# Kernel tuning notes

Measured on AMD Instinct MI355X. Metric: run time of the kernel, lower is better.

Reference implementation:

```python
import jax, jax.numpy as jnp
import numpy as np

N = 50000   # nodes
E = 1600000 # edges
D = 128     # feature dim (in = hidden = 128)


def setup_inputs() -> dict:
    key = jax.random.key(0)
    k1, k2, k3, k4 = jax.random.split(key, 4)
    scale = 1.0 / np.sqrt(D)
    return {
        "x": jax.random.normal(k1, (N, D), jnp.float32),
        "edge_index": jax.random.randint(k2, (2, E), 0, N, dtype=jnp.int32),
        "W0": jax.random.normal(k3, (D, D), jnp.float32) * scale,
        "b0": jnp.zeros((D,), jnp.float32),
        "W1": jax.random.normal(k4, (D, D), jnp.float32) * scale,
        "b1": jnp.zeros((D,), jnp.float32),
    }


def _gcn_norm(edge_index, num_nodes):
    # Add self-loops, compute symmetric normalization D^-1/2 A_hat D^-1/2.
    loop = jnp.arange(num_nodes, dtype=edge_index.dtype)
    src = jnp.concatenate([edge_index[0], loop])
    dst = jnp.concatenate([edge_index[1], loop])
    deg = jax.ops.segment_sum(jnp.ones_like(dst, jnp.float32), dst,
                              num_segments=num_nodes)
    dinv = jnp.where(deg > 0, jax.lax.rsqrt(deg), 0.0)
    norm = dinv[dst] * dinv[src]  # [E+N]
    return src, dst, norm


def _gcn_layer(x, src, dst, norm, W, b, num_nodes):
    h = x @ W                                  # [N, D]
    msg = h[src] * norm[:, None]               # gather + scale  [E+N, D]
    out = jax.ops.segment_sum(msg, dst, num_segments=num_nodes)  # scatter-add
    return out + b


def reference(x, edge_index, W0, b0, W1, b1):
    num_nodes = x.shape[0]
    src, dst, norm = _gcn_norm(edge_index, num_nodes)
    # forward loops over the first k=2 convs, ReLU after each (as in source)
    x = jax.nn.relu(_gcn_layer(x, src, dst, norm, W0, b0, num_nodes))
    x = jax.nn.relu(_gcn_layer(x, src, dst, norm, W1, b1, num_nodes))
    return x
```

## Files before the change

kernel.cpp:

```cpp
#include <hip/hip_runtime.h>
#include <hip/hip_bf16.h>

#define D 128
#define CHUNK 8192
#define SPAN_CAP 768


typedef __attribute__((ext_vector_type(8))) short short8;
typedef __attribute__((ext_vector_type(4))) float floatx4;

static __device__ inline unsigned int f2bf(float f) {
    unsigned int u = __float_as_uint(f);
    return (u + 0x7FFFu + ((u >> 16) & 1u)) >> 16;
}
static __device__ inline float bflo(unsigned int u) { return __uint_as_float(u << 16); }
static __device__ inline float bfhi(unsigned int u) { return __uint_as_float(u & 0xFFFF0000u); }

__global__ __launch_bounds__(256) void k01_swz_hist(const float* __restrict__ W0,
                                                    const float* __restrict__ W1,
                                                    short8* __restrict__ whi0, short8* __restrict__ wlo0,
                                                    short8* __restrict__ whi1, short8* __restrict__ wlo1,
                                                    const int* __restrict__ dst,
                                                    int* __restrict__ blockhist, int E_) {
    __shared__ int h[256];
    const int tid = threadIdx.x;
    if (blockIdx.x < 16) {
        int gid = blockIdx.x * 256 + tid;
        const float* W = (gid < 2048) ? W0 : W1;
        short8* whi = (gid < 2048) ? whi0 : whi1;
        short8* wlo = (gid < 2048) ? wlo0 : wlo1;
        int t2 = gid & 2047;
        int t = t2 >> 8, q = (t2 >> 6) & 3, lane = t2 & 63;
        short8 hi, lo;
        #pragma unroll
        for (int j = 0; j < 8; ++j) {
            int k = q * 32 + (lane >> 4) * 8 + j;
            int n = t * 16 + (lane & 15);
            float w = W[k * D + n];
            unsigned int hh = f2bf(w);
            hi[j] = (short)hh;
            lo[j] = (short)f2bf(w - __uint_as_float(hh << 16));
        }
        whi[t2] = hi;
        wlo[t2] = lo;
    } else {
        const int b = blockIdx.x - 16;
        h[tid] = 0;
        __syncthreads();
        const int e0 = b * CHUNK;
        const int e1 = min(E_, e0 + CHUNK);
        for (int e = e0 + tid; e < e1; e += 256)
            atomicAdd(&h[dst[e] >> 8], 1);
        __syncthreads();
        blockhist[b * 256 + tid] = h[tid];
    }
}

__global__ __launch_bounds__(256) void k23_scan_scatter(const int* __restrict__ blockhist,
                                                        const int* __restrict__ dst,
                                                        const int* __restrict__ src,
                                                        int* __restrict__ bucket_offs,
                                                        unsigned int* __restrict__ buf,
                                                        int NB, int NBUK, int E_) {
    __shared__ int s[256];
    __shared__ int c[256];
    const int myb = blockIdx.x, tid = threadIdx.x;
    int total = 0, prefix = 0;
    #pragma unroll 4
    for (int b2 = 0; b2 < NB; ++b2) {
        int t = blockhist[b2 * 256 + tid];
        total += t;
        prefix += (b2 < myb) ? t : 0;
    }
    s[tid] = total;
    __syncthreads();
    #pragma unroll
    for (int off = 1; off < 256; off <<= 1) {
        int x = (tid >= off) ? s[tid - off] : 0;
        __syncthreads();
        s[tid] += x;
        __syncthreads();
    }
    int bstart = s[tid] - total;
    if (myb == 0) {
        if (tid < NBUK) bucket_offs[tid] = bstart;
        if (tid == 0) bucket_offs[NBUK] = E_;
    }
    c[tid] = bstart + prefix;
    __syncthreads();

    const int e0 = myb * CHUNK;
    const int e1 = min(E_, e0 + CHUNK);
    for (int e = e0 + tid; e < e1; e += 256) {
        int v = dst[e];
        int sdx = src[e];
        int pos = atomicAdd(&c[v >> 8], 1);
        buf[pos] = (unsigned int)sdx | ((unsigned int)(v & 255) << 16);
    }
}

__global__ __launch_bounds__(256) void k4_bucket(const unsigned int* __restrict__ buf,
                                                 const int* __restrict__ bucket_offs,
                                                 int* __restrict__ offs,
                                                 float* __restrict__ dinv,
                                                 int* __restrict__ col, int N_, int E_) {
    __shared__ int h[256];
    __shared__ int s[256];
    __shared__ int c[256];
    const int beta = blockIdx.x, tid = threadIdx.x;
    const int start = bucket_offs[beta];
    const int end   = bucket_offs[beta + 1];

    h[tid] = 0;
    __syncthreads();
    for (int e = start + tid; e < end; e += 256)
        atomicAdd(&h[(buf[e] >> 16) & 255], 1);
    __syncthreads();

    int deg = h[tid];
    s[tid] = deg;
    __syncthreads();
    #pragma unroll
    for (int off = 1; off < 256; off <<= 1) {
        int x = (tid >= off) ? s[tid - off] : 0;
        __syncthreads();
        s[tid] += x;
        __syncthreads();
    }
    int excl = s[tid] - deg;

    int v0 = beta * 256 + tid;
    if (v0 < N_) {
        offs[v0] = start + excl;
        dinv[v0] = rsqrtf((float)(deg + 1));
    }
    if (beta == 0 && tid == 0) offs[N_] = E_;
    c[tid] = start + excl;
    __syncthreads();

    for (int e = start + tid; e < end; e += 256) {
        unsigned int p = buf[e];
        int pos = atomicAdd(&c[(p >> 16) & 255], 1);
        col[pos] = (int)(p & 0xFFFFu);
    }
}

__global__ __launch_bounds__(256) void gemm_mfma(const float* __restrict__ A,
                                                 const short8* __restrict__ whi,
                                                 const short8* __restrict__ wlo,
                                                 const float* __restrict__ dinv,
                                                 unsigned int* __restrict__ Gu, int nrows) {
    __shared__ float tileT[128][65];

    const int tid  = threadIdx.x;
    const int wave = tid >> 6, lane = tid & 63;
    const int m = lane & 15, quad = lane >> 4;
    const int rowInBlk = wave * 16;
    const int arow = min(blockIdx.x * 64 + rowInBlk + m, nrows - 1);
    const float* Ap = A + (size_t)arow * D + quad * 8;

    floatx4 acc[8];
    #pragma unroll
    for (int t = 0; t < 8; ++t) acc[t] = (floatx4){0.f, 0.f, 0.f, 0.f};

    #pragma unroll
    for (int q = 0; q < 4; ++q) {
        float4 a0 = *(const float4*)(Ap + q * 32);
        float4 a1 = *(const float4*)(Ap + q * 32 + 4);
        float av[8] = {a0.x, a0.y, a0.z, a0.w, a1.x, a1.y, a1.z, a1.w};
        short8 ahi, alo;
        #pragma unroll
        for (int j = 0; j < 8; ++j) {
            unsigned int h = f2bf(av[j]);
            ahi[j] = (short)h;
            alo[j] = (short)f2bf(av[j] - __uint_as_float(h << 16));
        }
        #pragma unroll
        for (int t = 0; t < 8; ++t) {
            short8 bh = whi[(t * 4 + q) * 64 + lane];
            short8 bl = wlo[(t * 4 + q) * 64 + lane];
            acc[t] = __builtin_amdgcn_mfma_f32_16x16x32_bf16(ahi, bh, acc[t], 0, 0, 0);
            acc[t] = __builtin_amdgcn_mfma_f32_16x16x32_bf16(alo, bh, acc[t], 0, 0, 0);
            acc[t] = __builtin_amdgcn_mfma_f32_16x16x32_bf16(ahi, bl, acc[t], 0, 0, 0);
        }
    }

    #pragma unroll
    for (int t = 0; t < 8; ++t)
        #pragma unroll
        for (int r = 0; r < 4; ++r)
            tileT[t * 16 + m][rowInBlk + quad * 4 + r] = acc[t][r];
    __syncthreads();

    const int orow = tid >> 2, seg = tid & 3;
    const int grow = blockIdx.x * 64 + orow;
    if (grow < nrows) {
        float s = dinv[grow];
        const int p = seg >> 1;
        unsigned int* Gp = Gu + ((size_t)(p * nrows + grow)) * 32 + (seg & 1) * 16;
        #pragma unroll
        for (int i = 0; i < 4; ++i) {
            int c0 = seg * 32 + i * 8;
            uint4 o4;
            o4.x = f2bf(tileT[c0 + 0][orow] * s) | (f2bf(tileT[c0 + 1][orow] * s) << 16);
            o4.y = f2bf(tileT[c0 + 2][orow] * s) | (f2bf(tileT[c0 + 3][orow] * s) << 16);
            o4.z = f2bf(tileT[c0 + 4][orow] * s) | (f2bf(tileT[c0 + 5][orow] * s) << 16);
            o4.w = f2bf(tileT[c0 + 6][orow] * s) | (f2bf(tileT[c0 + 7][orow] * s) << 16);
            ((uint4*)Gp)[i] = o4;
        }
    }
}

__global__ __launch_bounds__(256) void aggregate_kernel(const unsigned int* __restrict__ Gu,
                                                        const int* __restrict__ offs,
                                                        const int* __restrict__ col,
                                                        const float* __restrict__ dinv,
                                                        const float* __restrict__ bias,
                                                        float* __restrict__ out, int nnodes,
                                                        int ngroups) {
    __shared__ int scol[SPAN_CAP];
    __shared__ int soffs[9];
    const int bid   = blockIdx.x;
    const int xcd   = bid & 7;
    const int plane = xcd >> 2;
    const int i     = (bid >> 3) * 4 + (xcd & 3);
    if (i >= ngroups) return;
    const int tid   = threadIdx.x;
    const int node0 = i * 8;

    if (tid < 9) soffs[tid] = offs[min(node0 + tid, nnodes)];
    __syncthreads();
    const int s0   = soffs[0];
    const int span = soffs[8] - s0;
    const bool lds_ok = (span <= SPAN_CAP);
    if (lds_ok) {
        for (int k = tid; k < span; k += 256) scol[k] = col[s0 + k];
    }
    __syncthreads();

    const int lane = tid & 31;
    const int node = node0 + (tid >> 5);
    if (node >= nnodes) return;
    const unsigned int* P = Gu + (size_t)plane * nnodes * 32;

    unsigned int su = P[(size_t)node * 32 + lane];
    float ax = bflo(su), ay = bfhi(su);

    const int s = soffs[tid >> 5];
    const int e = soffs[(tid >> 5) + 1];
    int idx = s;

    if (lds_ok) {
        const int b0 = s - s0;
        int k = 0;
        const int deg = e - s;
        for (; k + 8 <= deg; k += 8) {
            int j0 = scol[b0 + k + 0], j1 = scol[b0 + k + 1], j2 = scol[b0 + k + 2], j3 = scol[b0 + k + 3];
            int j4 = scol[b0 + k + 4], j5 = scol[b0 + k + 5], j6 = scol[b0 + k + 6], j7 = scol[b0 + k + 7];
            unsigned int u0 = P[(size_t)j0 * 32 + lane];
            unsigned int u1 = P[(size_t)j1 * 32 + lane];
            unsigned int u2 = P[(size_t)j2 * 32 + lane];
            unsigned int u3 = P[(size_t)j3 * 32 + lane];
            unsigned int u4 = P[(size_t)j4 * 32 + lane];
            unsigned int u5 = P[(size_t)j5 * 32 + lane];
            unsigned int u6 = P[(size_t)j6 * 32 + lane];
            unsigned int u7 = P[(size_t)j7 * 32 + lane];
            ax += ((bflo(u0) + bflo(u1)) + (bflo(u2) + bflo(u3))) +
                  ((bflo(u4) + bflo(u5)) + (bflo(u6) + bflo(u7)));
            ay += ((bfhi(u0) + bfhi(u1)) + (bfhi(u2) + bfhi(u3))) +
                  ((bfhi(u4) + bfhi(u5)) + (bfhi(u6) + bfhi(u7)));
        }
        for (; k + 4 <= deg; k += 4) {
            int j0 = scol[b0 + k + 0], j1 = scol[b0 + k + 1], j2 = scol[b0 + k + 2], j3 = scol[b0 + k + 3];
            unsigned int u0 = P[(size_t)j0 * 32 + lane];
            unsigned int u1 = P[(size_t)j1 * 32 + lane];
            unsigned int u2 = P[(size_t)j2 * 32 + lane];
            unsigned int u3 = P[(size_t)j3 * 32 + lane];
            ax += (bflo(u0) + bflo(u1)) + (bflo(u2) + bflo(u3));
            ay += (bfhi(u0) + bfhi(u1)) + (bfhi(u2) + bfhi(u3));
        }
        for (; k < deg; ++k) {
            unsigned int u = P[(size_t)scol[b0 + k] * 32 + lane];
            ax += bflo(u);
            ay += bfhi(u);
        }
    } else {
        for (; idx + 4 <= e; idx += 4) {
            int j0 = col[idx + 0], j1 = col[idx + 1], j2 = col[idx + 2], j3 = col[idx + 3];
            unsigned int u0 = P[(size_t)j0 * 32 + lane];
            unsigned int u1 = P[(size_t)j1 * 32 + lane];
            unsigned int u2 = P[(size_t)j2 * 32 + lane];
            unsigned int u3 = P[(size_t)j3 * 32 + lane];
            ax += (bflo(u0) + bflo(u1)) + (bflo(u2) + bflo(u3));
            ay += (bfhi(u0) + bfhi(u1)) + (bfhi(u2) + bfhi(u3));
        }
        for (; idx < e; ++idx) {
            unsigned int u = P[(size_t)col[idx] * 32 + lane];
            ax += bflo(u);
            ay += bfhi(u);
        }
    }

    float dv = dinv[node];
    float2 bb = ((const float2*)bias)[plane * 32 + lane];
    float2 o;
    o.x = fmaxf(fmaf(dv, ax, bb.x), 0.f);
    o.y = fmaxf(fmaf(dv, ay, bb.y), 0.f);
    ((float2*)out)[(size_t)node * 64 + plane * 32 + lane] = o;
}

extern "C" void kernel_launch(void* const* d_in, const int* in_sizes, int n_in,
                              void* d_out, int out_size, void* d_ws, size_t ws_size,
                              hipStream_t stream) {
    const float* x    = (const float*)d_in[0];
    const int*   edge = (const int*)d_in[1];
    const float* W0   = (const float*)d_in[2];
    const float* b0   = (const float*)d_in[3];
    const float* W1   = (const float*)d_in[4];
    const float* b1   = (const float*)d_in[5];
    float* out = (float*)d_out;

    const int N_ = in_sizes[0] / D;
    const int E_ = in_sizes[1] / 2;
    const int* srcp = edge;
    const int* dstp = edge + E_;

    const int NB   = (E_ + CHUNK - 1) / CHUNK;
    const int NBUK = (N_ + 255) >> 8;

    char* p = (char*)d_ws;
    auto carve = [&](size_t bytes) { char* q = p; p += (bytes + 255) & ~(size_t)255; return q; };
    int*          blockhist = (int*)          carve((size_t)NB * 256 * 4);
    int*          buck_offs = (int*)          carve((size_t)(NBUK + 1) * 4);
    int*          offs      = (int*)          carve((size_t)(N_ + 1) * 4);
    float*        dinv      = (float*)        carve((size_t)N_ * 4);
    unsigned int* buf       = (unsigned int*) carve((size_t)E_ * 4);
    int*          col       = (int*)          carve((size_t)E_ * 4);
    unsigned int* gu        = (unsigned int*) carve((size_t)N_ * 64 * 4);
    short8*       whi0      = (short8*)       carve(2048 * 16);
    short8*       wlo0      = (short8*)       carve(2048 * 16);
    short8*       whi1      = (short8*)       carve(2048 * 16);
    short8*       wlo1      = (short8*)       carve(2048 * 16);

    k01_swz_hist   <<<16 + NB, 256, 0, stream>>>(W0, W1, whi0, wlo0, whi1, wlo1,
                                                 dstp, blockhist, E_);
    k23_scan_scatter<<<NB,     256, 0, stream>>>(blockhist, dstp, srcp, buck_offs, buf,
                                                 NB, NBUK, E_);
    k4_bucket      <<<NBUK,    256, 0, stream>>>(buf, buck_offs, offs, dinv, col, N_, E_);

    const int gmb = (N_ + 63) / 64;
    const int ngroups = (N_ + 7) / 8;
    const int agrid   = ((ngroups + 3) / 4) * 8;

    gemm_mfma       <<<gmb,   256, 0, stream>>>(x, whi0, wlo0, dinv, gu, N_);
    aggregate_kernel<<<agrid, 256, 0, stream>>>(gu, offs, col, dinv, b0, out, N_, ngroups);
    gemm_mfma       <<<gmb,   256, 0, stream>>>(out, whi1, wlo1, dinv, gu, N_);
    aggregate_kernel<<<agrid, 256, 0, stream>>>(gu, offs, col, dinv, b1, out, N_, ngroups);
}
```

Baseline: 258.7 us.

## Fuse CSR build kernels into one cooperative kernel with grid syncs

Merges the histogram, scan/scatter and per-bucket sort kernels into a single cooperative launch that uses grid-wide syncs. The per-block histogram table and serial cross-block prefix loop are replaced by one global 256-bucket histogram that blocks reserve ranges in with atomics. CHUNK shrinks so more blocks (16 + 782) share the edge work. The aim is to cut launch gaps and the O(NB) prefix reads, at the cost of grid-sync overhead and a requirement that all blocks be co-resident. Edge order within a bucket now depends on atomic order, so the CSR ordering is nondeterministic.

```diff
diff --git a/kernel.cpp b/kernel.cpp
--- a/kernel.cpp
+++ b/kernel.cpp
@@ -1,8 +1,11 @@
 #include <hip/hip_runtime.h>
 #include <hip/hip_bf16.h>
+#include <hip/hip_cooperative_groups.h>
+
+namespace cg = cooperative_groups;
 
 #define D 128
-#define CHUNK 8192
+#define CHUNK 2048
 #define SPAN_CAP 768
 
 
@@ -16,16 +19,31 @@
 static __device__ inline float bflo(unsigned int u) { return __uint_as_float(u << 16); }
 static __device__ inline float bfhi(unsigned int u) { return __uint_as_float(u & 0xFFFF0000u); }
 
-__global__ __launch_bounds__(256) void k01_swz_hist(const float* __restrict__ W0,
-                                                    const float* __restrict__ W1,
-                                                    short8* __restrict__ whi0, short8* __restrict__ wlo0,
-                                                    short8* __restrict__ whi1, short8* __restrict__ wlo1,
-                                                    const int* __restrict__ dst,
-                                                    int* __restrict__ blockhist, int E_) {
+__global__ __launch_bounds__(256) void k_build(const float* __restrict__ W0,
+                                               const float* __restrict__ W1,
+                                               short8* __restrict__ whi0, short8* __restrict__ wlo0,
+                                               short8* __restrict__ whi1, short8* __restrict__ wlo1,
+                                               const int* __restrict__ dst,
+                                               const int* __restrict__ src,
+                                               int* __restrict__ bhist,
+                                               unsigned int* __restrict__ buf,
+                                               int* __restrict__ col,
+                                               int* __restrict__ offs,
+                                               float* __restrict__ dinv,
+                                               int N_, int E_, int NB, int NBUK) {
+    cg::grid_group gg = cg::this_grid();
     __shared__ int h[256];
-    const int tid = threadIdx.x;
-    if (blockIdx.x < 16) {
-        int gid = blockIdx.x * 256 + tid;
+    __shared__ int myres[256];
+    __shared__ int s[256];
+    __shared__ int c[256];
+    const int bid = blockIdx.x, tid = threadIdx.x;
+    const bool isChunk = (bid >= 16);
+    const int chunk = bid - 16;
+    const int e0 = chunk * CHUNK;
+    const int e1 = min(E_, e0 + CHUNK);
+
+    if (bid < 16) {
+        int gid = bid * 256 + tid;
         const float* W = (gid < 2048) ? W0 : W1;
         short8* whi = (gid < 2048) ? whi0 : whi1;
         short8* wlo = (gid < 2048) ? wlo0 : wlo1;
@@ -44,104 +62,83 @@
         whi[t2] = hi;
         wlo[t2] = lo;
     } else {
-        const int b = blockIdx.x - 16;
+        if (bid == 16) bhist[tid] = 0;
         h[tid] = 0;
         __syncthreads();
-        const int e0 = b * CHUNK;
-        const int e1 = min(E_, e0 + CHUNK);
         for (int e = e0 + tid; e < e1; e += 256)
             atomicAdd(&h[dst[e] >> 8], 1);
         __syncthreads();
-        blockhist[b * 256 + tid] = h[tid];
-    }
-}
-
-__global__ __launch_bounds__(256) void k23_scan_scatter(const int* __restrict__ blockhist,
-                                                        const int* __restrict__ dst,
-                                                        const int* __restrict__ src,
-                                                        int* __restrict__ bucket_offs,
-                                                        unsigned int* __restrict__ buf,
-                                                        int NB, int NBUK, int E_) {
-    __shared__ int s[256];
-    __shared__ int c[256];
-    const int myb = blockIdx.x, tid = threadIdx.x;
-    int total = 0, prefix = 0;
-    #pragma unroll 4
-    for (int b2 = 0; b2 < NB; ++b2) {
-        int t = blockhist[b2 * 256 + tid];
-        total += t;
-        prefix += (b2 < myb) ? t : 0;
-    }
-    s[tid] = total;
-    __syncthreads();
-    #pragma unroll
-    for (int off = 1; off < 256; off <<= 1) {
-        int x = (tid >= off) ? s[tid - off] : 0;
-        __syncthreads();
-        s[tid] += x;
-        __syncthreads();
-    }
-    int bstart = s[tid] - total;
-    if (myb == 0) {
-        if (tid < NBUK) bucket_offs[tid] = bstart;
-        if (tid == 0) bucket_offs[NBUK] = E_;
-    }
-    c[tid] = bstart + prefix;
-    __syncthreads();
-
-    const int e0 = myb * CHUNK;
-    const int e1 = min(E_, e0 + CHUNK);
-    for (int e = e0 + tid; e < e1; e += 256) {
-        int v = dst[e];
-        int sdx = src[e];
-        int pos = atomicAdd(&c[v >> 8], 1);
-        buf[pos] = (unsigned int)sdx | ((unsigned int)(v & 255) << 16);
-    }
-}
-
-__global__ __launch_bounds__(256) void k4_bucket(const unsigned int* __restrict__ buf,
-                                                 const int* __restrict__ bucket_offs,
-                                                 int* __restrict__ offs,
-                                                 float* __restrict__ dinv,
-                                                 int* __restrict__ col, int N_, int E_) {
-    __shared__ int h[256];
-    __shared__ int s[256];
-    __shared__ int c[256];
-    const int beta = blockIdx.x, tid = threadIdx.x;
-    const int start = bucket_offs[beta];
-    const int end   = bucket_offs[beta + 1];
-
-    h[tid] = 0;
-    __syncthreads();
-    for (int e = start + tid; e < end; e += 256)
-        atomicAdd(&h[(buf[e] >> 16) & 255], 1);
-    __syncthreads();
-
-    int deg = h[tid];
-    s[tid] = deg;
-    __syncthreads();
-    #pragma unroll
-    for (int off = 1; off < 256; off <<= 1) {
-        int x = (tid >= off) ? s[tid - off] : 0;
-        __syncthreads();
-        s[tid] += x;
-        __syncthreads();
-    }
-    int excl = s[tid] - deg;
-
-    int v0 = beta * 256 + tid;
-    if (v0 < N_) {
-        offs[v0] = start + excl;
-        dinv[v0] = rsqrtf((float)(deg + 1));
-    }
-    if (beta == 0 && tid == 0) offs[N_] = E_;
-    c[tid] = start + excl;
-    __syncthreads();
-
-    for (int e = start + tid; e < end; e += 256) {
-        unsigned int p = buf[e];
-        int pos = atomicAdd(&c[(p >> 16) & 255], 1);
-        col[pos] = (int)(p & 0xFFFFu);
+    }
+    gg.sync();
+
+    if (isChunk) {
+        int cnt = h[tid];
+        myres[tid] = cnt ? atomicAdd(&bhist[tid], cnt) : 0;
+    }
+    gg.sync();
+
+    {
+        int t = bhist[tid];
+        s[tid] = t;
+        __syncthreads();
+        #pragma unroll
+        for (int off = 1; off < 256; off <<= 1) {
+            int x = (tid >= off) ? s[tid - off] : 0;
+            __syncthreads();
+            s[tid] += x;
+            __syncthreads();
+        }
+        if (isChunk) {
+            c[tid] = (s[tid] - t) + myres[tid];
+            __syncthreads();
+            for (int e = e0 + tid; e < e1; e += 256) {
+                int v = dst[e];
+                int sdx = src[e];
+                int beta = v >> 8;
+                int pos = atomicAdd(&c[beta], 1);
+                buf[pos] = (unsigned int)sdx | ((unsigned int)(v & 255) << 16);
+            }
+        }
+    }
+    gg.sync();
+
+    if (bid < NBUK) {
+        const int b_end   = s[bid];
+        const int b_cnt   = b_end - ((bid > 0) ? s[bid - 1] : 0);
+        const int b_start = b_end - b_cnt;
+
+        h[tid] = 0;
+        __syncthreads();
+        for (int e = b_start + tid; e < b_end; e += 256)
+            atomicAdd(&h[(buf[e] >> 16) & 255], 1);
+        __syncthreads();
+
+        int deg = h[tid];
+        c[tid] = deg;
+        __syncthreads();
+        #pragma unroll
+        for (int off = 1; off < 256; off <<= 1) {
+            int x = (tid >= off) ? c[tid - off] : 0;
+            __syncthreads();
+            c[tid] += x;
+            __syncthreads();
+        }
+        int excl = c[tid] - deg;
+
+        int v0 = bid * 256 + tid;
+        if (v0 < N_) {
+            offs[v0] = b_start + excl;
+            dinv[v0] = rsqrtf((float)(deg + 1));
+        }
+        if (bid == 0 && tid == 0) offs[N_] = E_;
+        myres[tid] = b_start + excl;
+        __syncthreads();
+
+        for (int e = b_start + tid; e < b_end; e += 256) {
+            unsigned int p = buf[e];
+            int pos = atomicAdd(&myres[(p >> 16) & 255], 1);
+            col[pos] = (int)(p & 0xFFFFu);
+        }
     }
 }
 
@@ -330,23 +327,27 @@
 
     char* p = (char*)d_ws;
     auto carve = [&](size_t bytes) { char* q = p; p += (bytes + 255) & ~(size_t)255; return q; };
-    int*          blockhist = (int*)          carve((size_t)NB * 256 * 4);
-    int*          buck_offs = (int*)          carve((size_t)(NBUK + 1) * 4);
-    int*          offs      = (int*)          carve((size_t)(N_ + 1) * 4);
-    float*        dinv      = (float*)        carve((size_t)N_ * 4);
-    unsigned int* buf       = (unsigned int*) carve((size_t)E_ * 4);
-    int*          col       = (int*)          carve((size_t)E_ * 4);
-    unsigned int* gu        = (unsigned int*) carve((size_t)N_ * 64 * 4);
-    short8*       whi0      = (short8*)       carve(2048 * 16);
-    short8*       wlo0      = (short8*)       carve(2048 * 16);
-    short8*       whi1      = (short8*)       carve(2048 * 16);
-    short8*       wlo1      = (short8*)       carve(2048 * 16);
-
-    k01_swz_hist   <<<16 + NB, 256, 0, stream>>>(W0, W1, whi0, wlo0, whi1, wlo1,
-                                                 dstp, blockhist, E_);
-    k23_scan_scatter<<<NB,     256, 0, stream>>>(blockhist, dstp, srcp, buck_offs, buf,
-                                                 NB, NBUK, E_);
-    k4_bucket      <<<NBUK,    256, 0, stream>>>(buf, buck_offs, offs, dinv, col, N_, E_);
+    int*          bhist  = (int*)          carve(256 * 4);
+    int*          offs   = (int*)          carve((size_t)(N_ + 1) * 4);
+    float*        dinv   = (float*)        carve((size_t)N_ * 4);
+    unsigned int* buf    = (unsigned int*) carve((size_t)E_ * 4);
+    int*          col    = (int*)          carve((size_t)E_ * 4);
+    unsigned int* gu     = (unsigned int*) carve((size_t)N_ * 64 * 4);
+    short8*       whi0   = (short8*)       carve(2048 * 16);
+    short8*       wlo0   = (short8*)       carve(2048 * 16);
+    short8*       whi1   = (short8*)       carve(2048 * 16);
+    short8*       wlo1   = (short8*)       carve(2048 * 16);
+
+    {
+        dim3 grid(16 + NB), blk(256);
+        void* args[] = {(void*)&W0, (void*)&W1,
+                        (void*)&whi0, (void*)&wlo0, (void*)&whi1, (void*)&wlo1,
+                        (void*)&dstp, (void*)&srcp,
+                        (void*)&bhist, (void*)&buf, (void*)&col,
+                        (void*)&offs, (void*)&dinv,
+                        (void*)&N_, (void*)&E_, (void*)&NB, (void*)&NBUK};
+        hipLaunchCooperativeKernel(reinterpret_cast<void*>(k_build), grid, blk, args, 0, stream);
+    }
 
     const int gmb = (N_ + 63) / 64;
     const int ngroups = (N_ + 7) / 8;
```

Result: slower. 496.4 us (+91.9%).
